# Performance work log

Hardware: AMD Instinct MI355X
Metric: run time of the kernel (lower is better)

The kernel has to match this reference:

```python
import jax, jax.numpy as jnp
import numpy as np

B, T, D = 2048, 200, 128


def setup_inputs() -> dict:
    key = jax.random.key(0)
    ks = jax.random.split(key, 6)
    query = jax.random.normal(ks[0], (B, D), dtype=jnp.float32)
    keys = jax.random.normal(ks[1], (B, T, D), dtype=jnp.float32)
    mask = jax.random.randint(ks[2], (B, T), 0, 2).astype(jnp.bool_)
    # nn.Linear(4D, D): weight [D, 4D], bias [D]
    lim1 = 1.0 / np.sqrt(4 * D)
    w1 = jax.random.uniform(ks[3], (D, 4 * D), minval=-lim1, maxval=lim1, dtype=jnp.float32)
    b1 = jnp.zeros((D,), dtype=jnp.float32)
    # PReLU single learnable slope (torch default init 0.25)
    prelu_a = jnp.asarray(0.25, dtype=jnp.float32)
    # nn.Linear(D, 1): weight [1, D] stored here as [D, 1], bias scalar
    lim2 = 1.0 / np.sqrt(D)
    w2 = jax.random.uniform(ks[4], (D, 1), minval=-lim2, maxval=lim2, dtype=jnp.float32)
    b2 = jnp.zeros((1,), dtype=jnp.float32)
    return {"query": query, "keys": keys, "mask": mask,
            "w1": w1, "b1": b1, "prelu_a": prelu_a, "w2": w2, "b2": b2}


def reference(query, keys, mask, w1, b1, prelu_a, w2, b2):
    # query: [B, D], keys: [B, T, D], mask: [B, T] bool
    q = jnp.broadcast_to(query[:, None, :], keys.shape)           # [B, T, D]
    x = jnp.concatenate([q, keys, q - keys, q * keys], axis=-1)   # [B, T, 4D]
    h = jnp.einsum('btf,df->btd', x, w1) + b1                     # [B, T, D]
    h = jnp.where(h >= 0, h, prelu_a * h)                         # PReLU
    scores = (h @ w2)[..., 0] + b2[0]                             # [B, T]
    scores = jnp.where(mask, scores, jnp.asarray(-1e9, scores.dtype))
    w = jax.nn.softmax(scores, axis=-1) * mask.astype(scores.dtype)
    w = w / jnp.maximum(w.sum(axis=-1, keepdims=True), 1e-6)
    return jnp.einsum('bt,btd->bd', w, keys)                      # [B, D]
```

## Files before the change

### kernel.cpp

```cpp
#include <hip/hip_runtime.h>

namespace {

constexpr int T  = 200;
constexpr int D  = 128;
constexpr int NT = 13;

typedef float f32x4 __attribute__((ext_vector_type(4)));
typedef short bf16x8 __attribute__((ext_vector_type(8)));

__device__ __forceinline__ short f2bf(float f) {
  unsigned u = __float_as_uint(f);
  return (short)((u + 0x7FFFu + ((u >> 16) & 1u)) >> 16);
}

constexpr int OFF_U2   = 8192;
constexpr int OFF_OUTL = 8448;
constexpr int OFF_RED  = 9472;
constexpr int SMEM_F   = 9488;

__global__ void pre_kernel(const float* __restrict__ w1, float* __restrict__ BmC,
                           float* __restrict__ Dm, float* __restrict__ sT) {
  int idx = blockIdx.x * 256 + threadIdx.x;
  int d = idx >> 7, f = idx & 127;
  const float* r = w1 + (size_t)d * 512;
  BmC[idx] = r[128 + f] - r[256 + f];
  Dm[idx]  = r[384 + f];
  sT[(size_t)f * 128 + d] = r[f] + r[256 + f];
}

__global__ __launch_bounds__(512, 4) void din_kernel(
    const float* __restrict__ qg, const float* __restrict__ keysg,
    const void* __restrict__ maskg, const float* __restrict__ w1g,
    const float* __restrict__ b1g, const float* __restrict__ pag,
    const float* __restrict__ w2g, const float* __restrict__ b2g,
    const float* __restrict__ BmC, const float* __restrict__ Dm,
    const float* __restrict__ sT, int usePre, float* __restrict__ outg) {
  __shared__ __align__(16) float smem[SMEM_F];
  float* u2   = smem + OFF_U2;
  float* outl = smem + OFF_OUTL;
  float* red  = smem + OFF_RED;

  const int tid  = threadIdx.x;
  const int b    = blockIdx.x;
  const int wid  = tid >> 6;
  const int lane = tid & 63;
  const int lrow = (lane >> 4) & 3;
  const int lcol = lane & 15;

  const float* qb    = qg + (size_t)b * D;
  const float* keysB = keysg + (size_t)b * T * D;

  int mcode;
  {
    unsigned v = ((const unsigned*)maskg)[lane];
    unsigned c0 = v & 255u, c1 = (v >> 8) & 255u, c2 = (v >> 16) & 255u, c3 = v >> 24;
    bool weird = (c0 == 0x80u) | (c0 == 0x3Fu) | (c1 == 0x80u) | (c1 == 0x3Fu) |
                 (c2 == 0x80u) | (c2 == 0x3Fu) | (c3 == 0x80u) | (c3 == 0x3Fu);
    bool nz = (v & 0xFFFFFF00u) != 0u;
    unsigned long long bw = __ballot(weird);
    unsigned long long bn = __ballot(nz);
    mcode = bw ? 2 : (bn ? 1 : 0);
  }

  const float pa  = pag[0];
  const float b2v = b2g[0];

  #pragma unroll
  for (int i = 0; i < 4; ++i) {
    int e = i * 4096 + tid * 8;
    int d = e >> 7, f = e & 127;
    f32x4 m0, m1, dd0, dd1;
    if (usePre) {
      m0  = *(const f32x4*)(BmC + e);  m1  = *(const f32x4*)(BmC + e + 4);
      dd0 = *(const f32x4*)(Dm + e);   dd1 = *(const f32x4*)(Dm + e + 4);
    } else {
      const float* r = w1g + (size_t)d * 512;
      f32x4 bB0 = *(const f32x4*)(r + 128 + f), bB1 = *(const f32x4*)(r + 128 + f + 4);
      f32x4 cC0 = *(const f32x4*)(r + 256 + f), cC1 = *(const f32x4*)(r + 256 + f + 4);
      m0 = bB0 - cC0; m1 = bB1 - cC1;
      dd0 = *(const f32x4*)(r + 384 + f); dd1 = *(const f32x4*)(r + 384 + f + 4);
    }
    f32x4 q0 = *(const f32x4*)(qb + f), q1 = *(const f32x4*)(qb + f + 4);
    bf16x8 v;
    v[0] = f2bf(m0.x + dd0.x * q0.x); v[1] = f2bf(m0.y + dd0.y * q0.y);
    v[2] = f2bf(m0.z + dd0.z * q0.z); v[3] = f2bf(m0.w + dd0.w * q0.w);
    v[4] = f2bf(m1.x + dd1.x * q1.x); v[5] = f2bf(m1.y + dd1.y * q1.y);
    v[6] = f2bf(m1.z + dd1.z * q1.z); v[7] = f2bf(m1.w + dd1.w * q1.w);
    int slot = (f >> 3) ^ (d & 15);
    *(bf16x8*)((char*)smem + d * 256 + slot * 16) = v;
  }

  if (tid < 256) {
    int d = tid & 127, fh = tid >> 7;
    float acc = 0.f;
    if (usePre) {
      const float* sp = sT + (size_t)(fh * 64) * 128 + d;
      const float* qh = qb + fh * 64;
      #pragma unroll
      for (int i = 0; i < 64; ++i) acc += qh[i] * sp[(size_t)i * 128];
    } else {
      const float* arow = w1g + (size_t)d * 512 + fh * 64;
      const float* crow = arow + 256;
      const float* qh   = qb + fh * 64;
      #pragma unroll
      for (int i = 0; i < 16; ++i) {
        f32x4 qv = *(const f32x4*)(qh + i * 4);
        f32x4 av = *(const f32x4*)(arow + i * 4);
        f32x4 cv = *(const f32x4*)(crow + i * 4);
        acc += qv.x * (av.x + cv.x) + qv.y * (av.y + cv.y) +
               qv.z * (av.z + cv.z) + qv.w * (av.w + cv.w);
      }
    }
    if (fh == 0) acc += b1g[d];
    u2[fh * 128 + d] = acc;
  }

  __syncthreads();

  float m_w = -1e9f, den_w = 0.f;
  float accpv[32];
  #pragma unroll
  for (int i = 0; i < 32; ++i) accpv[i] = 0.f;

  for (int rep = 0; rep < 2; ++rep) {
    int tile = wid + rep * 8;
    if (tile >= NT) break;
    int trow = tile * 16 + lcol;
    int trc  = trow < T ? trow : T - 1;

    const float* kr = keysB + (size_t)trc * D + lrow * 8;
    f32x4 k0[4], k1[4];
    #pragma unroll
    for (int ks = 0; ks < 4; ++ks) {
      k0[ks] = *(const f32x4*)(kr + ks * 32);
      k1[ks] = *(const f32x4*)(kr + ks * 32 + 4);
    }
    bf16x8 af[4];
    #pragma unroll
    for (int ks = 0; ks < 4; ++ks) {
      af[ks][0] = f2bf(k0[ks].x); af[ks][1] = f2bf(k0[ks].y);
      af[ks][2] = f2bf(k0[ks].z); af[ks][3] = f2bf(k0[ks].w);
      af[ks][4] = f2bf(k1[ks].x); af[ks][5] = f2bf(k1[ks].y);
      af[ks][6] = f2bf(k1[ks].z); af[ks][7] = f2bf(k1[ks].w);
    }

    float sj[4] = {0.f, 0.f, 0.f, 0.f};
    #pragma unroll
    for (int dt = 0; dt < 8; ++dt) {
      int d = dt * 16 + lcol;
      f32x4 acc = {0.f, 0.f, 0.f, 0.f};
      #pragma unroll
      for (int ks = 0; ks < 4; ++ks) {
        bf16x8 bfv = *(const bf16x8*)((const char*)smem + d * 256 +
                                      ((((ks * 4 + lrow)) ^ (d & 15)) << 4));
        acc = __builtin_amdgcn_mfma_f32_16x16x32_bf16(af[ks], bfv, acc, 0, 0, 0);
      }
      float u_d = u2[d] + u2[128 + d];
      float w2d = w2g[d];
      #pragma unroll
      for (int j = 0; j < 4; ++j) {
        float h = acc[j] + u_d;
        h = (h >= 0.f) ? h : pa * h;
        sj[j] += h * w2d;
      }
    }
    #pragma unroll
    for (int o = 1; o < 16; o <<= 1) {
      sj[0] += __shfl_xor(sj[0], o);
      sj[1] += __shfl_xor(sj[1], o);
      sj[2] += __shfl_xor(sj[2], o);
      sj[3] += __shfl_xor(sj[3], o);
    }
    float mt = -1e30f;
    #pragma unroll
    for (int j = 0; j < 4; ++j) {
      int t = tile * 16 + lrow * 4 + j;
      bool valid = (t < T);
      if (valid) {
        size_t mi = (size_t)b * T + t;
        if (mcode == 0)      valid = ((const int*)maskg)[mi] != 0;
        else if (mcode == 1) valid = ((const unsigned char*)maskg)[mi] != 0;
        else                 valid = ((const float*)maskg)[mi] != 0.f;
      }
      sj[j] = valid ? (sj[j] + b2v) : -1e30f;
      mt = fmaxf(mt, sj[j]);
    }
    mt = fmaxf(mt, __shfl_xor(mt, 16));
    mt = fmaxf(mt, __shfl_xor(mt, 32));

    float mnew  = fmaxf(m_w, mt);
    float scale = __expf(m_w - mnew);
    den_w *= scale;
    #pragma unroll
    for (int i = 0; i < 32; ++i) accpv[i] *= scale;
    m_w = mnew;

    float wj[4], dsum = 0.f;
    #pragma unroll
    for (int j = 0; j < 4; ++j) { wj[j] = __expf(sj[j] - mnew); dsum += wj[j]; }
    dsum += __shfl_xor(dsum, 16);
    dsum += __shfl_xor(dsum, 32);
    den_w += dsum;

    float tmp = (lcol & 2) ? ((lcol & 1) ? wj[3] : wj[2])
                           : ((lcol & 1) ? wj[1] : wj[0]);
    float wtr = __shfl(tmp, ((lcol >> 2) << 4) | (lcol & 3), 64);

    #pragma unroll
    for (int ks = 0; ks < 4; ++ks) {
      accpv[ks * 8 + 0] += wtr * k0[ks].x;
      accpv[ks * 8 + 1] += wtr * k0[ks].y;
      accpv[ks * 8 + 2] += wtr * k0[ks].z;
      accpv[ks * 8 + 3] += wtr * k0[ks].w;
      accpv[ks * 8 + 4] += wtr * k1[ks].x;
      accpv[ks * 8 + 5] += wtr * k1[ks].y;
      accpv[ks * 8 + 6] += wtr * k1[ks].z;
      accpv[ks * 8 + 7] += wtr * k1[ks].w;
    }
  }

  #pragma unroll
  for (int i = 0; i < 32; ++i) {
    float v = accpv[i];
    v += __shfl_xor(v, 1); v += __shfl_xor(v, 2);
    v += __shfl_xor(v, 4); v += __shfl_xor(v, 8);
    accpv[i] = v;
  }
  if (lcol == 0) {
    #pragma unroll
    for (int ks = 0; ks < 4; ++ks) {
      f32x4 a = {accpv[ks * 8 + 0], accpv[ks * 8 + 1], accpv[ks * 8 + 2], accpv[ks * 8 + 3]};
      f32x4 c = {accpv[ks * 8 + 4], accpv[ks * 8 + 5], accpv[ks * 8 + 6], accpv[ks * 8 + 7]};
      *(f32x4*)(outl + wid * 128 + ks * 32 + lrow * 8)     = a;
      *(f32x4*)(outl + wid * 128 + ks * 32 + lrow * 8 + 4) = c;
    }
  }
  if (lane == 0) { red[wid] = m_w; red[8 + wid] = den_w; }

  __syncthreads();

  if (tid < 128) {
    float M = red[0];
    #pragma unroll
    for (int w = 1; w < 8; ++w) M = fmaxf(M, red[w]);
    float den = 0.f, o = 0.f;
    #pragma unroll
    for (int w = 0; w < 8; ++w) {
      float scw = __expf(red[w] - M);
      den += red[8 + w] * scw;
      o   += outl[w * 128 + tid] * scw;
    }
    float inv = (den > 0.f) ? 1.0f / den : 0.f;
    outg[(size_t)b * D + tid] = o * inv;
  }
}

}

extern "C" void kernel_launch(void* const* d_in, const int* in_sizes, int n_in,
                              void* d_out, int out_size, void* d_ws, size_t ws_size,
                              hipStream_t stream) {
  (void)in_sizes; (void)n_in; (void)out_size;
  const float* q    = (const float*)d_in[0];
  const float* keys = (const float*)d_in[1];
  const void*  mask = d_in[2];
  const float* w1   = (const float*)d_in[3];
  const float* b1   = (const float*)d_in[4];
  const float* pa   = (const float*)d_in[5];
  const float* w2   = (const float*)d_in[6];
  const float* b2   = (const float*)d_in[7];
  float* out = (float*)d_out;

  float* ws = (float*)d_ws;
  int usePre = (ws_size >= (size_t)(3 * 16384) * sizeof(float)) ? 1 : 0;
  float* BmC = ws;
  float* Dm  = ws + 16384;
  float* sT  = ws + 32768;
  if (usePre) pre_kernel<<<64, 256, 0, stream>>>(w1, BmC, Dm, sT);
  din_kernel<<<2048, 512, 0, stream>>>(q, keys, mask, w1, b1, pa, w2, b2,
                                       BmC, Dm, sT, usePre, out);
}
```

Baseline: 85.80 us.

## Pack precomputed weights as bf16, halve block size, use DPP reductions

The precomputed weight tables are now stored as packed bf16 (the two matrices interleaved in one u32, the transposed sum as u16), halving workspace traffic per block. The block shrinks from 512 to 256 threads, so each wave handles up to four tiles instead of two. The 16-lane shuffles become DPP row adds, w2 is hoisted into registers, and the online-softmax rescale is skipped when the running max does not change. This trades less traffic and fewer shuffle instructions for extra bf16 rounding of weights and less parallelism per block.

```diff
diff --git a/kernel.cpp b/kernel.cpp
--- a/kernel.cpp
+++ b/kernel.cpp
@@ -1,4 +1,5 @@
 #include <hip/hip_runtime.h>
+#include <hip/hip_bf16.h>
 
 namespace {
 
@@ -8,34 +9,52 @@
 
 typedef float f32x4 __attribute__((ext_vector_type(4)));
 typedef short bf16x8 __attribute__((ext_vector_type(8)));
+typedef unsigned int u32;
+typedef u32 u32x4 __attribute__((ext_vector_type(4)));
 
 __device__ __forceinline__ short f2bf(float f) {
-  unsigned u = __float_as_uint(f);
-  return (short)((u + 0x7FFFu + ((u >> 16) & 1u)) >> 16);
+  __hip_bfloat16 h = __float2bfloat16(f);
+  return __builtin_bit_cast(short, h);
+}
+__device__ __forceinline__ float bflo2f(u32 u) { return __uint_as_float(u << 16); }
+__device__ __forceinline__ float bfhi2f(u32 u) { return __uint_as_float(u & 0xFFFF0000u); }
+
+template <int CTRL>
+__device__ __forceinline__ float dpp_add(float x) {
+  int y = __builtin_amdgcn_update_dpp(0, __float_as_int(x), CTRL, 0xF, 0xF, true);
+  return x + __int_as_float(y);
+}
+__device__ __forceinline__ float sum16(float x) {
+  x = dpp_add<0x121>(x);
+  x = dpp_add<0x122>(x);
+  x = dpp_add<0x124>(x);
+  x = dpp_add<0x128>(x);
+  return x;
 }
 
 constexpr int OFF_U2   = 8192;
 constexpr int OFF_OUTL = 8448;
-constexpr int OFF_RED  = 9472;
-constexpr int SMEM_F   = 9488;
-
-__global__ void pre_kernel(const float* __restrict__ w1, float* __restrict__ BmC,
-                           float* __restrict__ Dm, float* __restrict__ sT) {
+constexpr int OFF_RED  = 8960;
+constexpr int SMEM_F   = 8968;
+
+__global__ void pre_kernel(const float* __restrict__ w1, u32* __restrict__ MD,
+                           unsigned short* __restrict__ sTb) {
   int idx = blockIdx.x * 256 + threadIdx.x;
   int d = idx >> 7, f = idx & 127;
   const float* r = w1 + (size_t)d * 512;
-  BmC[idx] = r[128 + f] - r[256 + f];
-  Dm[idx]  = r[384 + f];
-  sT[(size_t)f * 128 + d] = r[f] + r[256 + f];
-}
-
-__global__ __launch_bounds__(512, 4) void din_kernel(
+  u32 lo = (unsigned short)f2bf(r[128 + f] - r[256 + f]);
+  u32 hi = (unsigned short)f2bf(r[384 + f]);
+  MD[idx] = lo | (hi << 16);
+  sTb[(size_t)f * 128 + d] = (unsigned short)f2bf(r[f] + r[256 + f]);
+}
+
+__global__ __launch_bounds__(256, 4) void din_kernel(
     const float* __restrict__ qg, const float* __restrict__ keysg,
     const void* __restrict__ maskg, const float* __restrict__ w1g,
     const float* __restrict__ b1g, const float* __restrict__ pag,
     const float* __restrict__ w2g, const float* __restrict__ b2g,
-    const float* __restrict__ BmC, const float* __restrict__ Dm,
-    const float* __restrict__ sT, int usePre, float* __restrict__ outg) {
+    const u32* __restrict__ MD, const unsigned short* __restrict__ sTb,
+    int usePre, float* __restrict__ outg) {
   __shared__ __align__(16) float smem[SMEM_F];
   float* u2   = smem + OFF_U2;
   float* outl = smem + OFF_OUTL;
@@ -66,39 +85,58 @@
   const float pa  = pag[0];
   const float b2v = b2g[0];
 
-  #pragma unroll
-  for (int i = 0; i < 4; ++i) {
-    int e = i * 4096 + tid * 8;
-    int d = e >> 7, f = e & 127;
-    f32x4 m0, m1, dd0, dd1;
-    if (usePre) {
-      m0  = *(const f32x4*)(BmC + e);  m1  = *(const f32x4*)(BmC + e + 4);
-      dd0 = *(const f32x4*)(Dm + e);   dd1 = *(const f32x4*)(Dm + e + 4);
-    } else {
+  if (usePre) {
+    #pragma unroll
+    for (int i = 0; i < 8; ++i) {
+      int e = i * 2048 + tid * 8;
+      int d = e >> 7, f = e & 127;
+      u32x4 A = *(const u32x4*)(MD + e);
+      u32x4 B = *(const u32x4*)(MD + e + 4);
+      f32x4 q0 = *(const f32x4*)(qb + f), q1 = *(const f32x4*)(qb + f + 4);
+      bf16x8 v;
+      v[0] = f2bf(bflo2f(A.x) + bfhi2f(A.x) * q0.x);
+      v[1] = f2bf(bflo2f(A.y) + bfhi2f(A.y) * q0.y);
+      v[2] = f2bf(bflo2f(A.z) + bfhi2f(A.z) * q0.z);
+      v[3] = f2bf(bflo2f(A.w) + bfhi2f(A.w) * q0.w);
+      v[4] = f2bf(bflo2f(B.x) + bfhi2f(B.x) * q1.x);
+      v[5] = f2bf(bflo2f(B.y) + bfhi2f(B.y) * q1.y);
+      v[6] = f2bf(bflo2f(B.z) + bfhi2f(B.z) * q1.z);
+      v[7] = f2bf(bflo2f(B.w) + bfhi2f(B.w) * q1.w);
+      int slot = (f >> 3) ^ (d & 15);
+      *(bf16x8*)((char*)smem + d * 256 + slot * 16) = v;
+    }
+  } else {
+    #pragma unroll
+    for (int i = 0; i < 8; ++i) {
+      int e = i * 2048 + tid * 8;
+      int d = e >> 7, f = e & 127;
       const float* r = w1g + (size_t)d * 512;
       f32x4 bB0 = *(const f32x4*)(r + 128 + f), bB1 = *(const f32x4*)(r + 128 + f + 4);
       f32x4 cC0 = *(const f32x4*)(r + 256 + f), cC1 = *(const f32x4*)(r + 256 + f + 4);
-      m0 = bB0 - cC0; m1 = bB1 - cC1;
-      dd0 = *(const f32x4*)(r + 384 + f); dd1 = *(const f32x4*)(r + 384 + f + 4);
-    }
-    f32x4 q0 = *(const f32x4*)(qb + f), q1 = *(const f32x4*)(qb + f + 4);
-    bf16x8 v;
-    v[0] = f2bf(m0.x + dd0.x * q0.x); v[1] = f2bf(m0.y + dd0.y * q0.y);
-    v[2] = f2bf(m0.z + dd0.z * q0.z); v[3] = f2bf(m0.w + dd0.w * q0.w);
-    v[4] = f2bf(m1.x + dd1.x * q1.x); v[5] = f2bf(m1.y + dd1.y * q1.y);
-    v[6] = f2bf(m1.z + dd1.z * q1.z); v[7] = f2bf(m1.w + dd1.w * q1.w);
-    int slot = (f >> 3) ^ (d & 15);
-    *(bf16x8*)((char*)smem + d * 256 + slot * 16) = v;
-  }
-
-  if (tid < 256) {
+      f32x4 dd0 = *(const f32x4*)(r + 384 + f), dd1 = *(const f32x4*)(r + 384 + f + 4);
+      f32x4 q0 = *(const f32x4*)(qb + f), q1 = *(const f32x4*)(qb + f + 4);
+      bf16x8 v;
+      v[0] = f2bf(bB0.x - cC0.x + dd0.x * q0.x);
+      v[1] = f2bf(bB0.y - cC0.y + dd0.y * q0.y);
+      v[2] = f2bf(bB0.z - cC0.z + dd0.z * q0.z);
+      v[3] = f2bf(bB0.w - cC0.w + dd0.w * q0.w);
+      v[4] = f2bf(bB1.x - cC1.x + dd1.x * q1.x);
+      v[5] = f2bf(bB1.y - cC1.y + dd1.y * q1.y);
+      v[6] = f2bf(bB1.z - cC1.z + dd1.z * q1.z);
+      v[7] = f2bf(bB1.w - cC1.w + dd1.w * q1.w);
+      int slot = (f >> 3) ^ (d & 15);
+      *(bf16x8*)((char*)smem + d * 256 + slot * 16) = v;
+    }
+  }
+
+  {
     int d = tid & 127, fh = tid >> 7;
     float acc = 0.f;
     if (usePre) {
-      const float* sp = sT + (size_t)(fh * 64) * 128 + d;
+      const unsigned short* sp = sTb + (size_t)(fh * 64) * 128 + d;
       const float* qh = qb + fh * 64;
       #pragma unroll
-      for (int i = 0; i < 64; ++i) acc += qh[i] * sp[(size_t)i * 128];
+      for (int i = 0; i < 64; ++i) acc += qh[i] * bflo2f(sp[(size_t)i * 128]);
     } else {
       const float* arow = w1g + (size_t)d * 512 + fh * 64;
       const float* crow = arow + 256;
@@ -112,20 +150,22 @@
                qv.z * (av.z + cv.z) + qv.w * (av.w + cv.w);
       }
     }
-    if (fh == 0) acc += b1g[d];
-    u2[fh * 128 + d] = acc;
+    if (fh == 0) acc += b1g[tid & 127];
+    u2[fh * 128 + (tid & 127)] = acc;
   }
 
   __syncthreads();
+
+  float w2w[8];
+  #pragma unroll
+  for (int dt = 0; dt < 8; ++dt) w2w[dt] = w2g[dt * 16 + lcol];
 
   float m_w = -1e9f, den_w = 0.f;
   float accpv[32];
   #pragma unroll
   for (int i = 0; i < 32; ++i) accpv[i] = 0.f;
 
-  for (int rep = 0; rep < 2; ++rep) {
-    int tile = wid + rep * 8;
-    if (tile >= NT) break;
+  for (int tile = wid; tile < NT; tile += 4) {
     int trow = tile * 16 + lcol;
     int trc  = trow < T ? trow : T - 1;
 
@@ -157,7 +197,7 @@
         acc = __builtin_amdgcn_mfma_f32_16x16x32_bf16(af[ks], bfv, acc, 0, 0, 0);
       }
       float u_d = u2[d] + u2[128 + d];
-      float w2d = w2g[d];
+      float w2d = w2w[dt];
       #pragma unroll
       for (int j = 0; j < 4; ++j) {
         float h = acc[j] + u_d;
@@ -166,12 +206,8 @@
       }
     }
     #pragma unroll
-    for (int o = 1; o < 16; o <<= 1) {
-      sj[0] += __shfl_xor(sj[0], o);
-      sj[1] += __shfl_xor(sj[1], o);
-      sj[2] += __shfl_xor(sj[2], o);
-      sj[3] += __shfl_xor(sj[3], o);
-    }
+    for (int j = 0; j < 4; ++j) sj[j] = sum16(sj[j]);
+
     float mt = -1e30f;
     #pragma unroll
     for (int j = 0; j < 4; ++j) {
@@ -189,16 +225,18 @@
     mt = fmaxf(mt, __shfl_xor(mt, 16));
     mt = fmaxf(mt, __shfl_xor(mt, 32));
 
-    float mnew  = fmaxf(m_w, mt);
-    float scale = __expf(m_w - mnew);
-    den_w *= scale;
-    #pragma unroll
-    for (int i = 0; i < 32; ++i) accpv[i] *= scale;
-    m_w = mnew;
+    float mnew = fmaxf(m_w, mt);
+    if (mnew > m_w) {
+      float sc = __expf(m_w - mnew);
+      den_w *= sc;
+      #pragma unroll
+      for (int i = 0; i < 32; ++i) accpv[i] *= sc;
+      m_w = mnew;
+    }
 
     float wj[4], dsum = 0.f;
     #pragma unroll
-    for (int j = 0; j < 4; ++j) { wj[j] = __expf(sj[j] - mnew); dsum += wj[j]; }
+    for (int j = 0; j < 4; ++j) { wj[j] = __expf(sj[j] - m_w); dsum += wj[j]; }
     dsum += __shfl_xor(dsum, 16);
     dsum += __shfl_xor(dsum, 32);
     den_w += dsum;
@@ -221,12 +259,7 @@
   }
 
   #pragma unroll
-  for (int i = 0; i < 32; ++i) {
-    float v = accpv[i];
-    v += __shfl_xor(v, 1); v += __shfl_xor(v, 2);
-    v += __shfl_xor(v, 4); v += __shfl_xor(v, 8);
-    accpv[i] = v;
-  }
+  for (int i = 0; i < 32; ++i) accpv[i] = sum16(accpv[i]);
   if (lcol == 0) {
     #pragma unroll
     for (int ks = 0; ks < 4; ++ks) {
@@ -236,19 +269,17 @@
       *(f32x4*)(outl + wid * 128 + ks * 32 + lrow * 8 + 4) = c;
     }
   }
-  if (lane == 0) { red[wid] = m_w; red[8 + wid] = den_w; }
+  if (lane == 0) { red[wid] = m_w; red[4 + wid] = den_w; }
 
   __syncthreads();
 
   if (tid < 128) {
-    float M = red[0];
-    #pragma unroll
-    for (int w = 1; w < 8; ++w) M = fmaxf(M, red[w]);
+    float M = fmaxf(fmaxf(red[0], red[1]), fmaxf(red[2], red[3]));
     float den = 0.f, o = 0.f;
     #pragma unroll
-    for (int w = 0; w < 8; ++w) {
+    for (int w = 0; w < 4; ++w) {
       float scw = __expf(red[w] - M);
-      den += red[8 + w] * scw;
+      den += red[4 + w] * scw;
       o   += outl[w * 128 + tid] * scw;
     }
     float inv = (den > 0.f) ? 1.0f / den : 0.f;
@@ -272,12 +303,10 @@
   const float* b2   = (const float*)d_in[7];
   float* out = (float*)d_out;
 
-  float* ws = (float*)d_ws;
-  int usePre = (ws_size >= (size_t)(3 * 16384) * sizeof(float)) ? 1 : 0;
-  float* BmC = ws;
-  float* Dm  = ws + 16384;
-  float* sT  = ws + 32768;
-  if (usePre) pre_kernel<<<64, 256, 0, stream>>>(w1, BmC, Dm, sT);
-  din_kernel<<<2048, 512, 0, stream>>>(q, keys, mask, w1, b1, pa, w2, b2,
-                                       BmC, Dm, sT, usePre, out);
-}
+  u32* MD = (u32*)d_ws;
+  unsigned short* sTb = (unsigned short*)((char*)d_ws + 65536);
+  int usePre = (ws_size >= (size_t)98304) ? 1 : 0;
+  if (usePre) pre_kernel<<<64, 256, 0, stream>>>(w1, MD, sTb);
+  din_kernel<<<2048, 256, 0, stream>>>(q, keys, mask, w1, b1, pa, w2, b2,
+                                       MD, sTb, usePre, out);
+}
```

Measured after the change: 227.7 us. +165.4%, slower.
